# Performance work log

Measured on AMD Instinct MI355X. Metric: run time of the kernel, lower is better.

## Reference

```python
import jax, jax.numpy as jnp
import numpy as np
import math

NUM_HEADS = 16
D_EMBED = 1024
D_HEAD = D_EMBED // NUM_HEADS


def setup_inputs() -> dict:
    key = jax.random.key(0)
    k1, k2, k3 = jax.random.split(key, 3)
    B, S = 4, 2048
    x = jax.random.normal(k1, (B, S, D_EMBED), dtype=jnp.float32)
    # Kaiming-ish init for the fused QKV and output projections
    scale_in = 1.0 / math.sqrt(D_EMBED)
    in_proj_weight = jax.random.normal(k2, (3 * D_EMBED, D_EMBED), dtype=jnp.float32) * scale_in
    out_proj_weight = jax.random.normal(k3, (D_EMBED, D_EMBED), dtype=jnp.float32) * scale_in
    return {
        "x": x,
        "in_proj_weight": in_proj_weight,
        "out_proj_weight": out_proj_weight,
        "causal_mask": 1,
    }


def reference(x, in_proj_weight, out_proj_weight, causal_mask):
    B, S, D = x.shape
    # fused QKV projection: x @ W_in^T -> [B, S, 3D], then split
    qkv = jnp.einsum("bsd,ed->bse", x, in_proj_weight)
    q, k, v = jnp.split(qkv, 3, axis=-1)
    # [B, S, H, dh] -> [B, H, S, dh]
    def to_heads(t):
        return t.reshape(B, S, NUM_HEADS, D_HEAD).transpose(0, 2, 1, 3)
    q, k, v = to_heads(q), to_heads(k), to_heads(v)
    # scores: [B, H, S, S]
    scores = jnp.einsum("bhqd,bhkd->bhqk", q, k) / math.sqrt(D_HEAD)
    if causal_mask:
        mask = jnp.triu(jnp.ones((S, S), dtype=bool), k=1)
        scores = jnp.where(mask, -jnp.inf, scores)
    attn = jax.nn.softmax(scores, axis=-1)
    out = jnp.einsum("bhqk,bhkd->bhqd", attn, v)
    out = out.transpose(0, 2, 1, 3).reshape(B, S, D)
    return jnp.einsum("bsd,ed->bse", out, out_proj_weight)
```

## Files before the change

### kernel.cpp

```cpp
#include <hip/hip_runtime.h>
#include <hip/hip_bf16.h>
#include <stdint.h>

typedef unsigned short u16;
typedef __attribute__((ext_vector_type(8))) short short8;
typedef __attribute__((ext_vector_type(4))) float floatx4;
typedef __attribute__((ext_vector_type(16))) float floatx16;
typedef __attribute__((ext_vector_type(4))) unsigned uint4v;
typedef __attribute__((ext_vector_type(2))) unsigned uint2v;

#define DEV static __device__ __forceinline__

DEV u16 f2bf(float f) {
  __hip_bfloat16 h = __float2bfloat16(f);
  return __builtin_bit_cast(u16, h);
}

DEV float fexp2(float x) {
  float r;
  asm("v_exp_f32 %0, %1" : "=v"(r) : "v"(x));
  return r;
}

DEV unsigned cvtpk(float lo, float hi) {
  unsigned r;
  asm("v_cvt_pk_bf16_f32 %0, %1, %2" : "=v"(r) : "v"(lo), "v"(hi));
  return r;
}

DEV void pswap(unsigned& a, unsigned& b) {
  uint2v r = __builtin_amdgcn_permlane32_swap(a, b, false, false);
  a = r[0];
  b = r[1];
}

DEV void cross32(float v, float& x, float& y) {
  unsigned a = __builtin_bit_cast(unsigned, v), b = a;
  pswap(a, b);
  x = __builtin_bit_cast(float, a);
  y = __builtin_bit_cast(float, b);
}

DEV floatx4 mfma16(short8 a, short8 b, floatx4 c) {
  return __builtin_amdgcn_mfma_f32_16x16x32_bf16(a, b, c, 0, 0, 0);
}
DEV floatx16 mfma32(short8 a, short8 b, floatx16 c) {
  return __builtin_amdgcn_mfma_f32_32x32x16_bf16(a, b, c, 0, 0, 0);
}

DEV void gload_lds16(const void* g, void* l) {
  __builtin_amdgcn_global_load_lds(
      (void __attribute__((address_space(1)))*)(g),
      (void __attribute__((address_space(3)))*)(l),
      16, 0, 0);
}

__global__ void cast_kernel(const float* __restrict__ in, u16* __restrict__ out, int n4) {
  int i = blockIdx.x * 256 + threadIdx.x;
  if (i >= n4) return;
  float4 v = reinterpret_cast<const float4*>(in)[i];
  ushort4 o;
  o.x = f2bf(v.x); o.y = f2bf(v.y); o.z = f2bf(v.z); o.w = f2bf(v.w);
  reinterpret_cast<ushort4*>(out)[i] = o;
}

template <int MODE>
__global__ __launch_bounds__(256, 2)
void gemm_bt(const u16* __restrict__ A, const u16* __restrict__ W,
             int M, int N, int K,
             u16* __restrict__ Qb, u16* __restrict__ Kb, u16* __restrict__ Vb,
             float* __restrict__ C) {
  __shared__ u16 As[2][128 * 32];
  __shared__ u16 Bs[2][128 * 32];
  const int tid = threadIdx.x;
  const int wave = tid >> 6, lane = tid & 63;
  const int lr = lane & 15, lg = lane >> 4;
  const int m0 = blockIdx.y * 128, n0 = blockIdx.x * 128;
  const int mq0 = (wave >> 1) * 64, nq0 = (wave & 1) * 64;
  const int srow = lane >> 2;
  const int sk8  = (lane & 3) * 8;

  floatx4 acc[4][4];
#pragma unroll
  for (int i = 0; i < 4; ++i)
#pragma unroll
    for (int j = 0; j < 4; ++j) acc[i][j] = (floatx4)0.f;

#pragma unroll
  for (int i = 0; i < 2; ++i) {
    int seg = wave + 4 * i;
    int r = seg * 16 + srow;
    gload_lds16(&A[(size_t)(m0 + r) * K + sk8], &As[0][seg * 512]);
    gload_lds16(&W[(size_t)(n0 + r) * K + sk8], &Bs[0][seg * 512]);
  }
  __syncthreads();

  int cur = 0;
  for (int kt = 0; kt < K; kt += 32) {
    if (kt + 32 < K) {
#pragma unroll
      for (int i = 0; i < 2; ++i) {
        int seg = wave + 4 * i;
        int r = seg * 16 + srow;
        gload_lds16(&A[(size_t)(m0 + r) * K + kt + 32 + sk8], &As[cur ^ 1][seg * 512]);
        gload_lds16(&W[(size_t)(n0 + r) * K + kt + 32 + sk8], &Bs[cur ^ 1][seg * 512]);
      }
    }

    short8 af[4], bf[4];
#pragma unroll
    for (int t = 0; t < 4; ++t)
      af[t] = *reinterpret_cast<const short8*>(&As[cur][(mq0 + t * 16 + lr) * 32 + lg * 8]);
#pragma unroll
    for (int t = 0; t < 4; ++t)
      bf[t] = *reinterpret_cast<const short8*>(&Bs[cur][(nq0 + t * 16 + lr) * 32 + lg * 8]);
#pragma unroll
    for (int i = 0; i < 4; ++i)
#pragma unroll
      for (int j = 0; j < 4; ++j)
        acc[i][j] = mfma16(af[i], bf[j], acc[i][j]);

    __syncthreads();
    cur ^= 1;
  }

  if (MODE == 0) {
#pragma unroll
    for (int j = 0; j < 4; ++j) {
      int n = n0 + nq0 + j * 16 + lr;
      int which = n >> 10;
      int d = n & 1023;
      int h = d >> 6, dh = d & 63;
      u16* dst = (which == 0) ? Qb : ((which == 1) ? Kb : Vb);
      float scale = (which == 0) ? 0.18033688f : 1.0f;
#pragma unroll
      for (int i = 0; i < 4; ++i) {
#pragma unroll
        for (int r = 0; r < 4; ++r) {
          int m = m0 + mq0 + i * 16 + lg * 4 + r;
          int b = m >> 11, s = m & 2047;
          dst[((size_t)(b * 16 + h) * 2048 + s) * 64 + dh] = f2bf(acc[i][j][r] * scale);
        }
      }
    }
  } else {
#pragma unroll
    for (int i = 0; i < 4; ++i)
#pragma unroll
      for (int j = 0; j < 4; ++j)
#pragma unroll
        for (int r = 0; r < 4; ++r) {
          int m = m0 + mq0 + i * 16 + lg * 4 + r;
          int n = n0 + nq0 + j * 16 + lr;
          C[(size_t)m * N + n] = acc[i][j][r];
        }
  }
}

__global__ __launch_bounds__(256, 2)
void attn_kernel(const u16* __restrict__ Qb, const u16* __restrict__ Kb,
                 const u16* __restrict__ Vb, u16* __restrict__ Ob) {
  const int bh = blockIdx.y;
  const u16* Qh = Qb + (size_t)bh * 2048 * 64;
  const u16* Kh = Kb + (size_t)bh * 2048 * 64;
  const u16* Vh = Vb + (size_t)bh * 2048 * 64;

  __shared__ u16 smem[2][8192];

  const int tid = threadIdx.x, wave = tid >> 6, lane = tid & 63;
  const int ln31 = lane & 31, hi = lane >> 5;
  const int swz = (lane & 7) * 8;
  const int b = bh >> 4, h = bh & 15;

  const int vp = tid & 31, vc8 = tid >> 5;

  for (int ph = 0; ph < 2; ++ph) {
    const int tq = ph ? (15 - (int)blockIdx.x) : (int)blockIdx.x;
    const int q0w = tq * 128 + wave * 32;
    const int qrow = q0w + ln31;

    short8 qf[4];
#pragma unroll
    for (int c = 0; c < 4; ++c)
      qf[c] = *reinterpret_cast<const short8*>(
          &Qh[(size_t)qrow * 64 + c * 16 + hi * 8]);

    floatx16 accO0 = (floatx16)0.f, accO1 = (floatx16)0.f;
    float m_run = -1e30f, l_run = 0.f;

    const int nt = 2 * (tq + 1);

    __syncthreads();
#pragma unroll
    for (int i = 0; i < 2; ++i) {
      int s = i * 256 + tid;
      int row = s >> 3;
      int col = ((s & 7) ^ (row & 7)) * 8;
      gload_lds16(&Kh[(size_t)row * 64 + col], &smem[0][(size_t)s * 8]);
    }
    {
      short8 v0 = *reinterpret_cast<const short8*>(&Vh[(size_t)(2 * vp) * 64 + vc8 * 8]);
      short8 v1 = *reinterpret_cast<const short8*>(&Vh[(size_t)(2 * vp + 1) * 64 + vc8 * 8]);
#pragma unroll
      for (int j = 0; j < 8; ++j) {
        int d = vc8 * 8 + j;
        uint32_t pk = (uint32_t)(u16)v0[j] | ((uint32_t)(u16)v1[j] << 16);
        *reinterpret_cast<uint32_t*>(&smem[0][4096 + d * 64 + ((2 * vp) ^ ((d & 7) * 8))]) = pk;
      }
    }
    __syncthreads();

    int cur = 0;
    for (int t = 0; t < nt; ++t) {
      const int kv0 = t * 64;
      const bool have_next = (t + 1 < nt);

      short8 nv0, nv1;
      if (have_next) {
        const int kvn = kv0 + 64;
#pragma unroll
        for (int i = 0; i < 2; ++i) {
          int s = i * 256 + tid;
          int row = s >> 3;
          int col = ((s & 7) ^ (row & 7)) * 8;
          gload_lds16(&Kh[(size_t)(kvn + row) * 64 + col], &smem[cur ^ 1][(size_t)s * 8]);
        }
        nv0 = *reinterpret_cast<const short8*>(&Vh[(size_t)(kvn + 2 * vp) * 64 + vc8 * 8]);
        nv1 = *reinterpret_cast<const short8*>(&Vh[(size_t)(kvn + 2 * vp + 1) * 64 + vc8 * 8]);
      }

      const u16* Ks = smem[cur];
      const u16* Vt = smem[cur] + 4096;

      if (kv0 <= q0w + 31) {
        floatx16 S0 = (floatx16)0.f, S1 = (floatx16)0.f;
        __builtin_amdgcn_s_setprio(1);
#pragma unroll
        for (int c = 0; c < 4; ++c) {
          short8 kfA = *reinterpret_cast<const short8*>(
              &Ks[ln31 * 64 + ((c * 16 + hi * 8) ^ swz)]);
          short8 kfB = *reinterpret_cast<const short8*>(
              &Ks[(32 + ln31) * 64 + ((c * 16 + hi * 8) ^ swz)]);
          S0 = mfma32(kfA, qf[c], S0);
          S1 = mfma32(kfB, qf[c], S1);
        }
        __builtin_amdgcn_s_setprio(0);
        if (kv0 + 63 > q0w) {
#pragma unroll
          for (int reg = 0; reg < 16; ++reg) {
            int kvA = kv0 + (reg & 3) + 8 * (reg >> 2) + 4 * hi;
            if (kvA > qrow) S0[reg] = -1e30f;
            if (kvA + 32 > qrow) S1[reg] = -1e30f;
          }
        }
        float m8[8];
#pragma unroll
        for (int i = 0; i < 8; ++i)
          m8[i] = fmaxf(fmaxf(S0[i], S0[i + 8]), fmaxf(S1[i], S1[i + 8]));
        float mx = fmaxf(fmaxf(fmaxf(m8[0], m8[1]), fmaxf(m8[2], m8[3])),
                         fmaxf(fmaxf(m8[4], m8[5]), fmaxf(m8[6], m8[7])));
        {
          float xa, xb;
          cross32(mx, xa, xb);
          mx = fmaxf(xa, xb);
        }
        bool small_ = (mx <= m_run + 8.f);
        if (!__all(small_)) {
          float mn = fmaxf(m_run, mx);
          float fac = fexp2(m_run - mn);
          m_run = mn;
          l_run *= fac;
          accO0 *= fac;
          accO1 *= fac;
        }
#pragma unroll
        for (int i = 0; i < 16; ++i) S0[i] = fexp2(S0[i] - m_run);
#pragma unroll
        for (int i = 0; i < 16; ++i) S1[i] = fexp2(S1[i] - m_run);
        float a8[8];
#pragma unroll
        for (int i = 0; i < 8; ++i)
          a8[i] = (S0[i] + S0[i + 8]) + (S1[i] + S1[i + 8]);
        float rs = ((a8[0] + a8[1]) + (a8[2] + a8[3])) + ((a8[4] + a8[5]) + (a8[6] + a8[7]));
        {
          float xa, xb;
          cross32(rs, xa, xb);
          rs = xa + xb;
        }
        l_run += rs;
        short8 pf[4];
#define BUILD_PF(idx, S, base)                                        \
        {                                                             \
          unsigned u01 = cvtpk(S[base + 0], S[base + 1]);             \
          unsigned u23 = cvtpk(S[base + 2], S[base + 3]);             \
          unsigned u45 = cvtpk(S[base + 4], S[base + 5]);             \
          unsigned u67 = cvtpk(S[base + 6], S[base + 7]);             \
          pswap(u01, u45);                                            \
          pswap(u23, u67);                                            \
          uint4v w; w.x = u01; w.y = u23; w.z = u45; w.w = u67;       \
          pf[idx] = __builtin_bit_cast(short8, w);                    \
        }
        BUILD_PF(0, S0, 0)
        BUILD_PF(1, S0, 8)
        BUILD_PF(2, S1, 0)
        BUILD_PF(3, S1, 8)
#undef BUILD_PF
        __builtin_amdgcn_s_setprio(1);
#pragma unroll
        for (int c = 0; c < 4; ++c) {
          short8 vfA = *reinterpret_cast<const short8*>(
              &Vt[ln31 * 64 + ((c * 16 + hi * 8) ^ swz)]);
          short8 vfB = *reinterpret_cast<const short8*>(
              &Vt[(32 + ln31) * 64 + ((c * 16 + hi * 8) ^ swz)]);
          accO0 = mfma32(vfA, pf[c], accO0);
          accO1 = mfma32(vfB, pf[c], accO1);
        }
        __builtin_amdgcn_s_setprio(0);
      }

      if (have_next) {
#pragma unroll
        for (int j = 0; j < 8; ++j) {
          int d = vc8 * 8 + j;
          uint32_t pk = (uint32_t)(u16)nv0[j] | ((uint32_t)(u16)nv1[j] << 16);
          *reinterpret_cast<uint32_t*>(
              &smem[cur ^ 1][4096 + d * 64 + ((2 * vp) ^ ((d & 7) * 8))]) = pk;
        }
      }
      __syncthreads();
      cur ^= 1;
    }

    u16* ep = &smem[0][0] + wave * 2048;
    float inv = 1.0f / l_run;
#define EPI_W(ACC, dh2)                                               \
    {                                                                 \
      _Pragma("unroll")                                               \
      for (int rp = 0; rp < 8; ++rp) {                                \
        int reg = rp * 2;                                             \
        unsigned pk = cvtpk(ACC[reg] * inv, ACC[reg + 1] * inv);      \
        int d = dh2 * 32 + (reg & 3) + 8 * (reg >> 2) + 4 * hi;       \
        *reinterpret_cast<uint32_t*>(                                 \
            &ep[ln31 * 64 + (d ^ ((ln31 & 7) * 8))]) = pk;            \
      }                                                               \
    }
    EPI_W(accO0, 0)
    EPI_W(accO1, 1)
#undef EPI_W
#pragma unroll
    for (int g = 0; g < 4; ++g) {
      int d0 = hi * 32 + g * 8;
      short8 o8 = *reinterpret_cast<const short8*>(
          &ep[ln31 * 64 + (d0 ^ ((ln31 & 7) * 8))]);
      *reinterpret_cast<short8*>(
          &Ob[(size_t)(b * 2048 + q0w + ln31) * 1024 + h * 64 + d0]) = o8;
    }
  }
}

extern "C" void kernel_launch(void* const* d_in, const int* in_sizes, int n_in,
                              void* d_out, int out_size, void* d_ws, size_t ws_size,
                              hipStream_t stream) {
  const float* x    = (const float*)d_in[0];
  const float* win  = (const float*)d_in[1];
  const float* wout = (const float*)d_in[2];
  float* out = (float*)d_out;

  char* ws = (char*)d_ws;
  u16* xb    = (u16*)(ws + 0);
  u16* winb  = (u16*)(ws + 16777216);
  u16* woutb = (u16*)(ws + 23068672);
  u16* Qb    = (u16*)(ws + 25165824);
  u16* Kb    = (u16*)(ws + 41943040);
  u16* Vb    = (u16*)(ws + 58720256);
  u16* Ob    = (u16*)(ws + 75497472);

  cast_kernel<<<8192, 256, 0, stream>>>(x, xb, 2097152);
  cast_kernel<<<3072, 256, 0, stream>>>(win, winb, 786432);
  cast_kernel<<<1024, 256, 0, stream>>>(wout, woutb, 262144);

  gemm_bt<0><<<dim3(24, 64), 256, 0, stream>>>(xb, winb, 8192, 3072, 1024,
                                               Qb, Kb, Vb, nullptr);
  attn_kernel<<<dim3(8, 64), 256, 0, stream>>>(Qb, Kb, Vb, Ob);
  gemm_bt<1><<<dim3(8, 64), 256, 0, stream>>>(Ob, woutb, 8192, 1024, 1024,
                                              nullptr, nullptr, nullptr, out);
}
```

Before: 185.2 us.

## Triple-buffer K/V tiles and software-pipeline QK^T ahead of softmax-PV

The attention kernel goes from double to triple LDS buffering, staging K/V two tiles ahead. The QK^T MFMAs for tile t+1 are issued before the softmax and PV of tile t, so matrix-core work can overlap the exp/reduction VALU phase. The cost is 48KB of shared memory per block instead of 32KB and more live score registers, which may reduce occupancy under launch_bounds(256,2).

```diff
diff --git a/kernel.cpp b/kernel.cpp
--- a/kernel.cpp
+++ b/kernel.cpp
@@ -165,7 +165,7 @@
   const u16* Kh = Kb + (size_t)bh * 2048 * 64;
   const u16* Vh = Vb + (size_t)bh * 2048 * 64;
 
-  __shared__ u16 smem[2][8192];
+  __shared__ u16 smem[3][8192];
 
   const int tid = threadIdx.x, wave = tid >> 6, lane = tid & 63;
   const int ln31 = lane & 31, hi = lane >> 5;
@@ -174,6 +174,28 @@
 
   const int vp = tid & 31, vc8 = tid >> 5;
 
+  auto stage_k = [&](int kvbase, u16* buf) {
+#pragma unroll
+    for (int i = 0; i < 2; ++i) {
+      int s = i * 256 + tid;
+      int row = s >> 3;
+      int col = ((s & 7) ^ (row & 7)) * 8;
+      gload_lds16(&Kh[(size_t)(kvbase + row) * 64 + col], &buf[(size_t)s * 8]);
+    }
+  };
+  auto load_v = [&](int kvbase, short8& v0, short8& v1) {
+    v0 = *reinterpret_cast<const short8*>(&Vh[(size_t)(kvbase + 2 * vp) * 64 + vc8 * 8]);
+    v1 = *reinterpret_cast<const short8*>(&Vh[(size_t)(kvbase + 2 * vp + 1) * 64 + vc8 * 8]);
+  };
+  auto write_v = [&](u16* buf, short8 v0, short8 v1) {
+#pragma unroll
+    for (int j = 0; j < 8; ++j) {
+      int d = vc8 * 8 + j;
+      uint32_t pk = (uint32_t)(u16)v0[j] | ((uint32_t)(u16)v1[j] << 16);
+      *reinterpret_cast<uint32_t*>(&buf[4096 + d * 64 + ((2 * vp) ^ ((d & 7) * 8))]) = pk;
+    }
+  };
+
   for (int ph = 0; ph < 2; ++ph) {
     const int tq = ph ? (15 - (int)blockIdx.x) : (int)blockIdx.x;
     const int q0w = tq * 128 + wave * 32;
@@ -188,147 +210,148 @@
     floatx16 accO0 = (floatx16)0.f, accO1 = (floatx16)0.f;
     float m_run = -1e30f, l_run = 0.f;
 
+    auto do_qk = [&](int kvq, floatx16& SQ0, floatx16& SQ1, const u16* Ksq) {
+      if (kvq > q0w + 31) return;
+      SQ0 = (floatx16)0.f;
+      SQ1 = (floatx16)0.f;
+      __builtin_amdgcn_s_setprio(1);
+#pragma unroll
+      for (int c = 0; c < 4; ++c) {
+        short8 kfA = *reinterpret_cast<const short8*>(
+            &Ksq[ln31 * 64 + ((c * 16 + hi * 8) ^ swz)]);
+        short8 kfB = *reinterpret_cast<const short8*>(
+            &Ksq[(32 + ln31) * 64 + ((c * 16 + hi * 8) ^ swz)]);
+        SQ0 = mfma32(kfA, qf[c], SQ0);
+        SQ1 = mfma32(kfB, qf[c], SQ1);
+      }
+      __builtin_amdgcn_s_setprio(0);
+    };
+
+    auto do_smpv = [&](int kv0_, floatx16& SS0, floatx16& SS1, const u16* bufv) {
+      if (kv0_ > q0w + 31) return;
+      if (kv0_ + 63 > q0w) {
+#pragma unroll
+        for (int reg = 0; reg < 16; ++reg) {
+          int kvA = kv0_ + (reg & 3) + 8 * (reg >> 2) + 4 * hi;
+          if (kvA > qrow) SS0[reg] = -1e30f;
+          if (kvA + 32 > qrow) SS1[reg] = -1e30f;
+        }
+      }
+      float m8[8];
+#pragma unroll
+      for (int i = 0; i < 8; ++i)
+        m8[i] = fmaxf(fmaxf(SS0[i], SS0[i + 8]), fmaxf(SS1[i], SS1[i + 8]));
+      float mx = fmaxf(fmaxf(fmaxf(m8[0], m8[1]), fmaxf(m8[2], m8[3])),
+                       fmaxf(fmaxf(m8[4], m8[5]), fmaxf(m8[6], m8[7])));
+      {
+        float xa, xb;
+        cross32(mx, xa, xb);
+        mx = fmaxf(xa, xb);
+      }
+      bool small_ = (mx <= m_run + 8.f);
+      if (!__all(small_)) {
+        float mn = fmaxf(m_run, mx);
+        float fac = fexp2(m_run - mn);
+        m_run = mn;
+        l_run *= fac;
+        accO0 *= fac;
+        accO1 *= fac;
+      }
+#pragma unroll
+      for (int i = 0; i < 16; ++i) SS0[i] = fexp2(SS0[i] - m_run);
+#pragma unroll
+      for (int i = 0; i < 16; ++i) SS1[i] = fexp2(SS1[i] - m_run);
+      float a8[8];
+#pragma unroll
+      for (int i = 0; i < 8; ++i)
+        a8[i] = (SS0[i] + SS0[i + 8]) + (SS1[i] + SS1[i + 8]);
+      float rs = ((a8[0] + a8[1]) + (a8[2] + a8[3])) + ((a8[4] + a8[5]) + (a8[6] + a8[7]));
+      {
+        float xa, xb;
+        cross32(rs, xa, xb);
+        rs = xa + xb;
+      }
+      l_run += rs;
+      short8 pf[4];
+#define BUILD_PF(idx, S, base)                                        \
+      {                                                               \
+        unsigned u01 = cvtpk(S[base + 0], S[base + 1]);               \
+        unsigned u23 = cvtpk(S[base + 2], S[base + 3]);               \
+        unsigned u45 = cvtpk(S[base + 4], S[base + 5]);               \
+        unsigned u67 = cvtpk(S[base + 6], S[base + 7]);               \
+        pswap(u01, u45);                                              \
+        pswap(u23, u67);                                              \
+        uint4v w; w.x = u01; w.y = u23; w.z = u45; w.w = u67;         \
+        pf[idx] = __builtin_bit_cast(short8, w);                      \
+      }
+      BUILD_PF(0, SS0, 0)
+      BUILD_PF(1, SS0, 8)
+      BUILD_PF(2, SS1, 0)
+      BUILD_PF(3, SS1, 8)
+#undef BUILD_PF
+      const u16* Vt = bufv + 4096;
+      __builtin_amdgcn_s_setprio(1);
+#pragma unroll
+      for (int c = 0; c < 4; ++c) {
+        short8 vfA = *reinterpret_cast<const short8*>(
+            &Vt[ln31 * 64 + ((c * 16 + hi * 8) ^ swz)]);
+        short8 vfB = *reinterpret_cast<const short8*>(
+            &Vt[(32 + ln31) * 64 + ((c * 16 + hi * 8) ^ swz)]);
+        accO0 = mfma32(vfA, pf[c], accO0);
+        accO1 = mfma32(vfB, pf[c], accO1);
+      }
+      __builtin_amdgcn_s_setprio(0);
+    };
+
     const int nt = 2 * (tq + 1);
 
     __syncthreads();
-#pragma unroll
-    for (int i = 0; i < 2; ++i) {
-      int s = i * 256 + tid;
-      int row = s >> 3;
-      int col = ((s & 7) ^ (row & 7)) * 8;
-      gload_lds16(&Kh[(size_t)row * 64 + col], &smem[0][(size_t)s * 8]);
-    }
+    stage_k(0, smem[0]);
     {
-      short8 v0 = *reinterpret_cast<const short8*>(&Vh[(size_t)(2 * vp) * 64 + vc8 * 8]);
-      short8 v1 = *reinterpret_cast<const short8*>(&Vh[(size_t)(2 * vp + 1) * 64 + vc8 * 8]);
-#pragma unroll
-      for (int j = 0; j < 8; ++j) {
-        int d = vc8 * 8 + j;
-        uint32_t pk = (uint32_t)(u16)v0[j] | ((uint32_t)(u16)v1[j] << 16);
-        *reinterpret_cast<uint32_t*>(&smem[0][4096 + d * 64 + ((2 * vp) ^ ((d & 7) * 8))]) = pk;
-      }
+      short8 v0, v1;
+      load_v(0, v0, v1);
+      write_v(smem[0], v0, v1);
+    }
+    stage_k(64, smem[1]);
+    {
+      short8 v0, v1;
+      load_v(64, v0, v1);
+      write_v(smem[1], v0, v1);
     }
     __syncthreads();
 
-    int cur = 0;
-    for (int t = 0; t < nt; ++t) {
-      const int kv0 = t * 64;
-      const bool have_next = (t + 1 < nt);
-
-      short8 nv0, nv1;
-      if (have_next) {
-        const int kvn = kv0 + 64;
-#pragma unroll
-        for (int i = 0; i < 2; ++i) {
-          int s = i * 256 + tid;
-          int row = s >> 3;
-          int col = ((s & 7) ^ (row & 7)) * 8;
-          gload_lds16(&Kh[(size_t)(kvn + row) * 64 + col], &smem[cur ^ 1][(size_t)s * 8]);
+    floatx16 SA0, SA1, SB0, SB1;
+    do_qk(0, SA0, SA1, smem[0]);
+
+    for (int it = 0; it < nt; it += 2) {
+      {
+        const int kvc = it * 64;
+        short8 nv0, nv1;
+        const bool do_st = (it + 2) < nt;
+        u16* sbuf = smem[(it + 2) % 3];
+        if (do_st) {
+          stage_k(kvc + 128, sbuf);
+          load_v(kvc + 128, nv0, nv1);
         }
-        nv0 = *reinterpret_cast<const short8*>(&Vh[(size_t)(kvn + 2 * vp) * 64 + vc8 * 8]);
-        nv1 = *reinterpret_cast<const short8*>(&Vh[(size_t)(kvn + 2 * vp + 1) * 64 + vc8 * 8]);
-      }
-
-      const u16* Ks = smem[cur];
-      const u16* Vt = smem[cur] + 4096;
-
-      if (kv0 <= q0w + 31) {
-        floatx16 S0 = (floatx16)0.f, S1 = (floatx16)0.f;
-        __builtin_amdgcn_s_setprio(1);
-#pragma unroll
-        for (int c = 0; c < 4; ++c) {
-          short8 kfA = *reinterpret_cast<const short8*>(
-              &Ks[ln31 * 64 + ((c * 16 + hi * 8) ^ swz)]);
-          short8 kfB = *reinterpret_cast<const short8*>(
-              &Ks[(32 + ln31) * 64 + ((c * 16 + hi * 8) ^ swz)]);
-          S0 = mfma32(kfA, qf[c], S0);
-          S1 = mfma32(kfB, qf[c], S1);
+        do_qk(kvc + 64, SB0, SB1, smem[(it + 1) % 3]);
+        do_smpv(kvc, SA0, SA1, smem[it % 3]);
+        if (do_st) write_v(sbuf, nv0, nv1);
+        __syncthreads();
+      }
+      {
+        const int kvc = it * 64 + 64;
+        short8 nv0, nv1;
+        const bool do_st = (it + 3) < nt;
+        u16* sbuf = smem[(it + 3) % 3];
+        if (do_st) {
+          stage_k(kvc + 128, sbuf);
+          load_v(kvc + 128, nv0, nv1);
         }
-        __builtin_amdgcn_s_setprio(0);
-        if (kv0 + 63 > q0w) {
-#pragma unroll
-          for (int reg = 0; reg < 16; ++reg) {
-            int kvA = kv0 + (reg & 3) + 8 * (reg >> 2) + 4 * hi;
-            if (kvA > qrow) S0[reg] = -1e30f;
-            if (kvA + 32 > qrow) S1[reg] = -1e30f;
-          }
-        }
-        float m8[8];
-#pragma unroll
-        for (int i = 0; i < 8; ++i)
-          m8[i] = fmaxf(fmaxf(S0[i], S0[i + 8]), fmaxf(S1[i], S1[i + 8]));
-        float mx = fmaxf(fmaxf(fmaxf(m8[0], m8[1]), fmaxf(m8[2], m8[3])),
-                         fmaxf(fmaxf(m8[4], m8[5]), fmaxf(m8[6], m8[7])));
-        {
-          float xa, xb;
-          cross32(mx, xa, xb);
-          mx = fmaxf(xa, xb);
-        }
-        bool small_ = (mx <= m_run + 8.f);
-        if (!__all(small_)) {
-          float mn = fmaxf(m_run, mx);
-          float fac = fexp2(m_run - mn);
-          m_run = mn;
-          l_run *= fac;
-          accO0 *= fac;
-          accO1 *= fac;
-        }
-#pragma unroll
-        for (int i = 0; i < 16; ++i) S0[i] = fexp2(S0[i] - m_run);
-#pragma unroll
-        for (int i = 0; i < 16; ++i) S1[i] = fexp2(S1[i] - m_run);
-        float a8[8];
-#pragma unroll
-        for (int i = 0; i < 8; ++i)
-          a8[i] = (S0[i] + S0[i + 8]) + (S1[i] + S1[i + 8]);
-        float rs = ((a8[0] + a8[1]) + (a8[2] + a8[3])) + ((a8[4] + a8[5]) + (a8[6] + a8[7]));
-        {
-          float xa, xb;
-          cross32(rs, xa, xb);
-          rs = xa + xb;
-        }
-        l_run += rs;
-        short8 pf[4];
-#define BUILD_PF(idx, S, base)                                        \
-        {                                                             \
-          unsigned u01 = cvtpk(S[base + 0], S[base + 1]);             \
-          unsigned u23 = cvtpk(S[base + 2], S[base + 3]);             \
-          unsigned u45 = cvtpk(S[base + 4], S[base + 5]);             \
-          unsigned u67 = cvtpk(S[base + 6], S[base + 7]);             \
-          pswap(u01, u45);                                            \
-          pswap(u23, u67);                                            \
-          uint4v w; w.x = u01; w.y = u23; w.z = u45; w.w = u67;       \
-          pf[idx] = __builtin_bit_cast(short8, w);                    \
-        }
-        BUILD_PF(0, S0, 0)
-        BUILD_PF(1, S0, 8)
-        BUILD_PF(2, S1, 0)
-        BUILD_PF(3, S1, 8)
-#undef BUILD_PF
-        __builtin_amdgcn_s_setprio(1);
-#pragma unroll
-        for (int c = 0; c < 4; ++c) {
-          short8 vfA = *reinterpret_cast<const short8*>(
-              &Vt[ln31 * 64 + ((c * 16 + hi * 8) ^ swz)]);
-          short8 vfB = *reinterpret_cast<const short8*>(
-              &Vt[(32 + ln31) * 64 + ((c * 16 + hi * 8) ^ swz)]);
-          accO0 = mfma32(vfA, pf[c], accO0);
-          accO1 = mfma32(vfB, pf[c], accO1);
-        }
-        __builtin_amdgcn_s_setprio(0);
-      }
-
-      if (have_next) {
-#pragma unroll
-        for (int j = 0; j < 8; ++j) {
-          int d = vc8 * 8 + j;
-          uint32_t pk = (uint32_t)(u16)nv0[j] | ((uint32_t)(u16)nv1[j] << 16);
-          *reinterpret_cast<uint32_t*>(
-              &smem[cur ^ 1][4096 + d * 64 + ((2 * vp) ^ ((d & 7) * 8))]) = pk;
-        }
-      }
-      __syncthreads();
-      cur ^= 1;
+        if (it + 2 < nt) do_qk(kvc + 64, SA0, SA1, smem[(it + 2) % 3]);
+        do_smpv(kvc, SB0, SB1, smem[(it + 1) % 3]);
+        if (do_st) write_v(sbuf, nv0, nv1);
+        __syncthreads();
+      }
     }
 
     u16* ep = &smem[0][0] + wave * 2048;
```

Result: no change. 182.4 us (-1.5%).
